# Kernel tuning notes

Measured on AMD Instinct MI355X. Metric: run time of the kernel, lower is better.

The kernel has to match this reference:

```python
import jax, jax.numpy as jnp
import numpy as np


def _conv(x, w, b):
    # NCHW conv with 'same' padding derived from kernel size (matches nn.Conv2d padding=k//2)
    ph, pw = w.shape[2] // 2, w.shape[3] // 2
    y = jax.lax.conv_general_dilated(
        x, w, window_strides=(1, 1), padding=[(ph, ph), (pw, pw)],
        dimension_numbers=("NCHW", "OIHW", "NCHW"))
    return y + b[None, :, None, None]


def _attn(q, k, v):
    # q,k,v: [N,C,H,W]; spatial self-attention over S=H*W positions
    N, C, H, W = q.shape
    S = H * W
    qf = q.reshape(N, C, S)
    kf = k.reshape(N, C, S)
    vf = v.reshape(N, C, S)
    scores = jnp.einsum("ncs,nct->nst", qf, kf) / jnp.sqrt(jnp.asarray(C, qf.dtype))
    a = jax.nn.softmax(scores, axis=-1)
    z = jnp.einsum("nst,nct->ncs", a, vf)
    return z.reshape(N, C, H, W)


def setup_inputs() -> dict:
    key = jax.random.key(0)
    ks = jax.random.split(key, 14)
    B, T, Ci, Hd, H, W = 4, 10, 1, 64, 32, 32
    sc = 0.05
    return {
        "x": jax.random.uniform(ks[0], (B, T, Ci, H, W), jnp.float32),
        # SAConvLSTMCell main conv: (Ci+Hd) -> 4*Hd, 3x3
        "w_conv": jax.random.normal(ks[1], (4 * Hd, Ci + Hd, 3, 3), jnp.float32) * sc,
        "b_conv": jax.random.normal(ks[2], (4 * Hd,), jnp.float32) * sc,
        # SA conv_h: Hd -> 3*Hd, 1x1
        "w_h": jax.random.normal(ks[3], (3 * Hd, Hd, 1, 1), jnp.float32) * sc,
        "b_h": jax.random.normal(ks[4], (3 * Hd,), jnp.float32) * sc,
        # SA conv_m: Hd -> 2*Hd, 1x1
        "w_m": jax.random.normal(ks[5], (2 * Hd, Hd, 1, 1), jnp.float32) * sc,
        "b_m": jax.random.normal(ks[6], (2 * Hd,), jnp.float32) * sc,
        # SA conv_z: 2*Hd -> Hd, 1x1
        "w_z": jax.random.normal(ks[7], (Hd, 2 * Hd, 1, 1), jnp.float32) * sc,
        "b_z": jax.random.normal(ks[8], (Hd,), jnp.float32) * sc,
        # SA conv_output: 2*Hd -> 3*Hd, 3x3
        "w_sa": jax.random.normal(ks[9], (3 * Hd, 2 * Hd, 3, 3), jnp.float32) * sc,
        "b_sa": jax.random.normal(ks[10], (3 * Hd,), jnp.float32) * sc,
        # conv_out: Hd -> Ci, 1x1
        "w_co": jax.random.normal(ks[11], (Ci, Hd, 1, 1), jnp.float32) * sc,
        "b_co": jax.random.normal(ks[12], (Ci,), jnp.float32) * sc,
        "future_frames": 10,
    }


def reference(x, w_conv, b_conv, w_h, b_h, w_m, b_m, w_z, b_z,
              w_sa, b_sa, w_co, b_co, future_frames):
    B, T, Ci, H, W = x.shape
    Hd = w_conv.shape[0] // 4

    def cell(xt, h, c, m):
        cc = _conv(jnp.concatenate([xt, h], axis=1), w_conv, b_conv)
        i, f, o, g = jnp.split(cc, 4, axis=1)
        c_new = jax.nn.sigmoid(f) * c + jax.nn.sigmoid(i) * jnp.tanh(g)
        h_cur = jax.nn.sigmoid(o) * jnp.tanh(c_new)
        # spatial self-attention memory update
        hq, hk, hv = jnp.split(_conv(h_cur, w_h, b_h), 3, axis=1)
        mk, mv = jnp.split(_conv(m, w_m, b_m), 2, axis=1)
        Zh = _attn(hq, hk, hv)
        Zm = _attn(hq, mk, mv)
        Z = _conv(jnp.concatenate([Zh, Zm], axis=1), w_z, b_z)
        i2, g2, o2 = jnp.split(_conv(jnp.concatenate([Z, h_cur], axis=1), w_sa, b_sa), 3, axis=1)
        i2 = jax.nn.sigmoid(i2)
        m_new = i2 * jnp.tanh(g2) + (1.0 - i2) * m
        h_new = jax.nn.sigmoid(o2) * m_new
        return h_new, c_new, m_new

    z = jnp.zeros((B, Hd, H, W), x.dtype)
    state0 = (z, z, z)

    def enc_step(carry, xt):
        h, c, m = carry
        return cell(xt, h, c, m), None

    (h, c, m), _ = jax.lax.scan(enc_step, state0, jnp.moveaxis(x, 1, 0))

    # first decoder input: raw conv_out(h) (no sigmoid, per the original code path)
    inp0 = _conv(h, w_co, b_co)

    def dec_step(carry, _):
        h, c, m, inp = carry
        h, c, m = cell(inp, h, c, m)
        pred = jax.nn.sigmoid(_conv(h, w_co, b_co))
        return (h, c, m, pred), pred

    _, preds = jax.lax.scan(dec_step, (h, c, m, inp0), None, length=future_frames)
    return jnp.moveaxis(preds, 0, 1)  # [B, future_frames, Ci, H, W]
```

## Files before the change

kernel.cpp:

```cpp
#include <hip/hip_runtime.h>
#include <math.h>

#define SS 1024

typedef unsigned short u16;
typedef __attribute__((ext_vector_type(8))) __bf16 bf16x8;
typedef __attribute__((ext_vector_type(4))) float f32x4;

#define MFMA(a,b,c) __builtin_amdgcn_mfma_f32_16x16x32_bf16(a,b,c,0,0,0)

__device__ __forceinline__ float sigm(float x){ return 1.f/(1.f+__expf(-x)); }
__device__ __forceinline__ u16 f2b(float x){ return __builtin_bit_cast(u16,(__bf16)x); }
__device__ __forceinline__ float b2f(u16 u){ return (float)__builtin_bit_cast(__bf16,u); }
__device__ __forceinline__ bf16x8 ldb8(const u16* p){ return *(const bf16x8*)p; }
__device__ __forceinline__ void st4b(u16* p, const f32x4 v){
  union { u16 u[4]; uint2 w; } t;
  t.u[0]=f2b(v[0]); t.u[1]=f2b(v[1]); t.u[2]=f2b(v[2]); t.u[3]=f2b(v[3]);
  *(uint2*)p = t.w;
}

__global__ __launch_bounds__(256) void k_prep(
    const float* __restrict__ wconv, const float* __restrict__ wh,
    const float* __restrict__ wm, const float* __restrict__ wz,
    const float* __restrict__ wsa,
    u16* __restrict__ Wg, u16* __restrict__ Whm,
    u16* __restrict__ Wzp, u16* __restrict__ Wsap)
{
  const int idx = blockIdx.x*256 + threadIdx.x;
  if (idx < 155648) {
    const int step = idx >> 13, co = (idx >> 5) & 255, j = idx & 31;
    float v = 0.f;
    if (step < 18) {
      const int tap = step >> 1, ci = 1 + (step & 1)*32 + j;
      v = wconv[co*585 + ci*9 + tap];
    } else if (j < 9) {
      v = wconv[co*585 + j];
    }
    Wg[idx] = f2b(v);
    return;
  }
  int l = idx - 155648;
  if (l < 20480) {
    const int step = l / 10240, row = (l >> 5) % 320, j = l & 31;
    const int ci = step*32 + j;
    const float v = (row < 192) ? wh[row*64+ci]*(row < 64 ? 0.125f : 1.f)
                                : wm[(row-192)*64+ci];
    Whm[l] = f2b(v);
    return;
  }
  l -= 20480;
  if (l < 8192) {
    const int step = l >> 11, co = (l >> 5) & 63, j = l & 31;
    Wzp[l] = f2b(wz[co*128 + step*32 + j]);
    return;
  }
  l -= 8192;
  if (l < 221184) {
    const int step = l / 6144, co = (l >> 5) % 192, j = l & 31;
    const int tap = step >> 2, ci = (step & 3)*32 + j;
    Wsap[l] = f2b(wsa[(co*128+ci)*9 + tap]);
  }
}

__global__ __launch_bounds__(256) void k_A(
    const u16* __restrict__ hTb, const float* __restrict__ xsrc, int xbs,
    const u16* __restrict__ Wg, const float* __restrict__ bconv,
    float* __restrict__ cT, u16* __restrict__ xcat,
    const u16* __restrict__ mTb, const u16* __restrict__ Whm,
    const float* __restrict__ bh, const float* __restrict__ bm,
    u16* __restrict__ qT, u16* __restrict__ kT, u16* __restrict__ mkT,
    u16* __restrict__ vC, u16* __restrict__ mvC)
{
  __shared__ u16 hcl[16][72];
  const int b = blockIdx.y, s0 = blockIdx.x*16;
  const int tid = threadIdx.x, wid = tid>>6, lane = tid&63, gl = lane>>4, n = lane&15;
  const u16* hb = hTb + (size_t)b*SS*64;
  const int s = s0 + n, y = s>>5, x = s&31;
  f32x4 acc[4];
#pragma unroll
  for (int g4 = 0; g4 < 4; ++g4) {
    const int co = g4*64 + wid*16 + gl*4;
    acc[g4] = (f32x4){ bconv[co], bconv[co+1], bconv[co+2], bconv[co+3] };
  }
  bf16x8 xb;
  {
    union { u16 u[8]; bf16x8 v; } t;
#pragma unroll
    for (int j = 0; j < 8; ++j) t.u[j] = 0;
    if (gl == 0) {
#pragma unroll
      for (int j = 0; j < 8; ++j) {
        const int dy = j/3 - 1, dx = j%3 - 1;
        if ((unsigned)(y+dy) < 32u && (unsigned)(x+dx) < 32u)
          t.u[j] = f2b(xsrc[b*xbs + s + dy*32 + dx]);
      }
    } else if (gl == 1) {
      if (y+1 < 32 && x+1 < 32) t.u[0] = f2b(xsrc[b*xbs + s + 33]);
    }
    xb = t.v;
  }
#pragma unroll
  for (int step = 0; step < 18; ++step) {
    const int tap = step>>1, half = step&1;
    const int dy = tap/3 - 1, dx = tap%3 - 1;
    const bool ok = ((unsigned)(y+dy) < 32u) & ((unsigned)(x+dx) < 32u);
    const int sc = ok ? (s + dy*32 + dx) : s;
    bf16x8 bv = ldb8(hb + (size_t)sc*64 + half*32 + gl*8);
    bv = ok ? bv : (bf16x8){};
#pragma unroll
    for (int g4 = 0; g4 < 4; ++g4) {
      const bf16x8 a = ldb8(Wg + step*8192 + (g4*64 + wid*16 + n)*32 + gl*8);
      acc[g4] = MFMA(a, bv, acc[g4]);
    }
  }
#pragma unroll
  for (int g4 = 0; g4 < 4; ++g4) {
    const bf16x8 a = ldb8(Wg + 18*8192 + (g4*64 + wid*16 + n)*32 + gl*8);
    acc[g4] = MFMA(a, xb, acc[g4]);
  }
  const int hd0 = wid*16 + gl*4;
  {
    float* cp = cT + ((size_t)b*SS + s)*64 + hd0;
    f32x4 cv = *(f32x4*)cp, hcv;
#pragma unroll
    for (int rr = 0; rr < 4; ++rr) {
      const float cn = sigm(acc[1][rr])*cv[rr] + sigm(acc[0][rr])*tanhf(acc[3][rr]);
      cv[rr] = cn;
      hcv[rr] = sigm(acc[2][rr])*tanhf(cn);
    }
    *(f32x4*)cp = cv;
    st4b(xcat + ((size_t)b*SS + s)*128 + 64 + hd0, hcv);
    st4b(&hcl[n][hd0], hcv);
  }
  __syncthreads();
  const int r0 = wid*16, cb = r0 + gl*4;
  f32x4 a1[5];
  a1[0] = (f32x4){ bh[cb]*0.125f, bh[cb+1]*0.125f, bh[cb+2]*0.125f, bh[cb+3]*0.125f };
  a1[1] = (f32x4){ bh[64+cb], bh[64+cb+1], bh[64+cb+2], bh[64+cb+3] };
  a1[2] = (f32x4){ bh[128+cb], bh[128+cb+1], bh[128+cb+2], bh[128+cb+3] };
  a1[3] = (f32x4){ bm[cb], bm[cb+1], bm[cb+2], bm[cb+3] };
  a1[4] = (f32x4){ bm[64+cb], bm[64+cb+1], bm[64+cb+2], bm[64+cb+3] };
#pragma unroll
  for (int step = 0; step < 2; ++step) {
    const bf16x8 bhc = ldb8(&hcl[n][step*32 + gl*8]);
    const bf16x8 bmm = ldb8(mTb + ((size_t)b*SS+s)*64 + step*32 + gl*8);
#pragma unroll
    for (int tt = 0; tt < 5; ++tt) {
      const bf16x8 a = ldb8(Whm + step*10240 + (tt*64 + r0 + n)*32 + gl*8);
      a1[tt] = MFMA(a, tt < 3 ? bhc : bmm, a1[tt]);
    }
  }
  const size_t ps = ((size_t)b*SS + s)*64 + cb;
  st4b(qT + ps, a1[0]);
  st4b(kT + ps, a1[1]);
  st4b(mkT + ps, a1[3]);
#pragma unroll
  for (int rr = 0; rr < 4; ++rr) {
    vC[((size_t)b*64 + cb + rr)*SS + s] = f2b(a1[2][rr]);
    mvC[((size_t)b*64 + cb + rr)*SS + s] = f2b(a1[4][rr]);
  }
}

__global__ __launch_bounds__(256) void k_B(
    const u16* __restrict__ qT, const u16* __restrict__ kT,
    const u16* __restrict__ mkT, const u16* __restrict__ vC,
    const u16* __restrict__ mvC,
    const u16* __restrict__ Wzp, const float* __restrict__ bz,
    u16* __restrict__ xcat)
{
  __shared__ u16 ldsP[4*16*72];
  __shared__ float oS[2][16][65];
  __shared__ float mS[2][16], lS[2][16];
  __shared__ u16 zbuf[16][136];
  const int tid = threadIdx.x, wid = tid>>6, lane = tid&63, gl = lane>>4, n = lane&15;
  const int b = blockIdx.z ? 0 : blockIdx.y, s0 = blockIdx.x*16;
  const int at = wid & 1, kv = wid >> 1;
  const u16* qb = qT + (size_t)b*SS*64;
  const u16* kb = (at ? mkT : kT) + (size_t)b*SS*64;
  const u16* vb = (at ? mvC : vC) + (size_t)b*64*SS;
  const bf16x8 bq0 = ldb8(qb + (size_t)(s0+n)*64 + gl*8);
  const bf16x8 bq1 = ldb8(qb + (size_t)(s0+n)*64 + 32 + gl*8);
  f32x4 o[4];
#pragma unroll
  for (int ct = 0; ct < 4; ++ct) o[ct] = (f32x4){0.f,0.f,0.f,0.f};
  float mrun = -1e30f, lrun = 0.f;
  u16* pb = ldsP + wid*1152 + n*72;

  for (int step = 0; step < 8; ++step) {
    const int t0 = kv*512 + step*64;
    f32x4 st4[4];
#pragma unroll
    for (int tt = 0; tt < 4; ++tt) {
      const u16* kr = kb + (size_t)(t0 + tt*16 + n)*64;
      f32x4 a = {0.f,0.f,0.f,0.f};
      a = MFMA(ldb8(kr + gl*8), bq0, a);
      a = MFMA(ldb8(kr + 32 + gl*8), bq1, a);
      st4[tt] = a;
    }
    float mt = -1e30f;
#pragma unroll
    for (int tt = 0; tt < 4; ++tt)
#pragma unroll
      for (int rr = 0; rr < 4; ++rr) mt = fmaxf(mt, st4[tt][rr]);
    mt = fmaxf(mt, __shfl_xor(mt, 16));
    mt = fmaxf(mt, __shfl_xor(mt, 32));
    const float mnew = fmaxf(mrun, mt);
    const float f = __expf(mrun - mnew);
    float ps = 0.f;
#pragma unroll
    for (int tt = 0; tt < 4; ++tt) {
      const float p0e = __expf(st4[tt][0]-mnew), p1e = __expf(st4[tt][1]-mnew);
      const float p2e = __expf(st4[tt][2]-mnew), p3e = __expf(st4[tt][3]-mnew);
      ps += (p0e + p1e) + (p2e + p3e);
      *(unsigned*)(pb + tt*16 + gl*4)     = (unsigned)f2b(p0e) | ((unsigned)f2b(p1e)<<16);
      *(unsigned*)(pb + tt*16 + gl*4 + 2) = (unsigned)f2b(p2e) | ((unsigned)f2b(p3e)<<16);
    }
    ps += __shfl_xor(ps, 16);
    ps += __shfl_xor(ps, 32);
    lrun = lrun*f + ps;
    mrun = mnew;
    float fr[4];
#pragma unroll
    for (int rr = 0; rr < 4; ++rr) fr[rr] = __shfl(f, gl*4 + rr);
#pragma unroll
    for (int ct = 0; ct < 4; ++ct)
#pragma unroll
      for (int rr = 0; rr < 4; ++rr) o[ct][rr] *= fr[rr];
    const bf16x8 pa0 = ldb8(pb + gl*8);
    const bf16x8 pa1 = ldb8(pb + 32 + gl*8);
#pragma unroll
    for (int ct = 0; ct < 4; ++ct) {
      const u16* vr = vb + (size_t)(ct*16 + n)*SS + t0;
      o[ct] = MFMA(pa0, ldb8(vr + gl*8), o[ct]);
      o[ct] = MFMA(pa1, ldb8(vr + 32 + gl*8), o[ct]);
    }
  }
  if (kv == 1) {
#pragma unroll
    for (int ct = 0; ct < 4; ++ct)
#pragma unroll
      for (int rr = 0; rr < 4; ++rr) oS[at][gl*4+rr][ct*16+n] = o[ct][rr];
    if (gl == 0) { mS[at][n] = mrun; lS[at][n] = lrun; }
  }
  __syncthreads();
  if (kv == 0) {
    const float m1 = mS[at][n], l1 = lS[at][n];
    const float mm = fmaxf(mrun, m1);
    const float e0 = __expf(mrun - mm), e1 = __expf(m1 - mm);
    const float inv = 1.f / (lrun*e0 + l1*e1);
    const float a0 = e0*inv, a1v = e1*inv;
    float f0r[4], f1r[4];
#pragma unroll
    for (int rr = 0; rr < 4; ++rr) {
      f0r[rr] = __shfl(a0, gl*4 + rr);
      f1r[rr] = __shfl(a1v, gl*4 + rr);
    }
#pragma unroll
    for (int ct = 0; ct < 4; ++ct)
#pragma unroll
      for (int rr = 0; rr < 4; ++rr)
        zbuf[gl*4+rr][at*64 + ct*16 + n] =
            f2b(o[ct][rr]*f0r[rr] + oS[at][gl*4+rr][ct*16+n]*f1r[rr]);
  }
  __syncthreads();
  const int co = wid*16 + gl*4;
  f32x4 acc = (f32x4){ bz[co], bz[co+1], bz[co+2], bz[co+3] };
#pragma unroll
  for (int qq = 0; qq < 4; ++qq) {
    const bf16x8 bv = ldb8(&zbuf[n][qq*32 + gl*8]);
    const bf16x8 a = ldb8(Wzp + qq*2048 + (wid*16 + n)*32 + gl*8);
    acc = MFMA(a, bv, acc);
  }
  st4b(xcat + ((size_t)b*SS + s0 + n)*128 + co, acc);
}

__global__ __launch_bounds__(256) void k_C(
    const u16* __restrict__ xcat, const u16* __restrict__ Wsap,
    const float* __restrict__ bsa,
    float* __restrict__ mT, u16* __restrict__ mTb, u16* __restrict__ hTb,
    const float* __restrict__ wco, const float* __restrict__ bco,
    float* __restrict__ inp, float* __restrict__ out, int mode, int j)
{
  __shared__ float pool[16][17];
  const int b = blockIdx.y, s0 = blockIdx.x*16;
  const int tid = threadIdx.x, wid = tid>>6, lane = tid&63, gl = lane>>4, n = lane&15;
  const int hd0 = wid*16 + gl*4;
  const int s = s0 + n, y = s>>5, x = s&31;
  f32x4 acc[3];
#pragma unroll
  for (int i = 0; i < 3; ++i) {
    const int co = i*64 + hd0;
    acc[i] = (f32x4){ bsa[co], bsa[co+1], bsa[co+2], bsa[co+3] };
  }
#pragma unroll
  for (int step = 0; step < 36; ++step) {
    const int tap = step>>2, qq = step&3;
    const int dy = tap/3 - 1, dx = tap%3 - 1;
    const bool ok = ((unsigned)(y+dy) < 32u) & ((unsigned)(x+dx) < 32u);
    const int sc = ok ? (s + dy*32 + dx) : s;
    bf16x8 bv = ldb8(xcat + ((size_t)b*SS + sc)*128 + qq*32 + gl*8);
    bv = ok ? bv : (bf16x8){};
#pragma unroll
    for (int i = 0; i < 3; ++i) {
      const bf16x8 a = ldb8(Wsap + step*6144 + (i*64 + wid*16 + n)*32 + gl*8);
      acc[i] = MFMA(a, bv, acc[i]);
    }
  }
  float* mp = mT + ((size_t)b*SS + s)*64 + hd0;
  f32x4 mv4 = *(f32x4*)mp, hv;
#pragma unroll
  for (int rr = 0; rr < 4; ++rr) {
    const float i2 = sigm(acc[0][rr]);
    const float mn = i2*tanhf(acc[1][rr]) + (1.f - i2)*mv4[rr];
    mv4[rr] = mn;
    hv[rr] = sigm(acc[2][rr])*mn;
  }
  *(f32x4*)mp = mv4;
  st4b(mTb + ((size_t)b*SS + s)*64 + hd0, mv4);
  st4b(hTb + ((size_t)b*SS + s)*64 + hd0, hv);
  if (mode >= 0) {
    pool[n][wid*4 + gl] = hv[0]*wco[hd0] + hv[1]*wco[hd0+1]
                        + hv[2]*wco[hd0+2] + hv[3]*wco[hd0+3];
    __syncthreads();
    if (tid < 16) {
      float v = bco[0];
#pragma unroll
      for (int i = 0; i < 16; ++i) v += pool[tid][i];
      const int sp = s0 + tid;
      if (mode == 1) {
        v = sigm(v);
        out[((size_t)b*10 + j)*SS + sp] = v;
      }
      inp[b*SS + sp] = v;
    }
  }
}

extern "C" void kernel_launch(void* const* d_in, const int* in_sizes, int n_in,
                              void* d_out, int out_size, void* d_ws, size_t ws_size,
                              hipStream_t stream) {
  const float* x      = (const float*)d_in[0];
  const float* w_conv = (const float*)d_in[1];
  const float* b_conv = (const float*)d_in[2];
  const float* w_h    = (const float*)d_in[3];
  const float* b_h    = (const float*)d_in[4];
  const float* w_m    = (const float*)d_in[5];
  const float* b_m    = (const float*)d_in[6];
  const float* w_z    = (const float*)d_in[7];
  const float* b_z    = (const float*)d_in[8];
  const float* w_sa   = (const float*)d_in[9];
  const float* b_sa   = (const float*)d_in[10];
  const float* w_co   = (const float*)d_in[11];
  const float* b_co   = (const float*)d_in[12];
  float* out = (float*)d_out;

  float* ws  = (float*)d_ws;
  float* cT  = ws;
  float* mT  = ws + 262144;
  float* inp = ws + 524288;
  u16* ub   = (u16*)(ws + 528384);
  u16* hTb  = ub;
  u16* mTb  = ub + 262144;
  u16* xcat = ub + 524288;
  u16* qT   = ub + 1048576;
  u16* kT   = ub + 1310720;
  u16* mkT  = ub + 1572864;
  u16* vC   = ub + 1835008;
  u16* mvC  = ub + 2097152;
  u16* Wg   = ub + 2359296;
  u16* Whm  = ub + 2514944;
  u16* Wzp  = ub + 2535424;
  u16* Wsap = ub + 2543616;

  hipMemsetAsync(ws, 0, (size_t)524288*4, stream);
  hipMemsetAsync(hTb, 0, (size_t)524288*2, stream);
  k_prep<<<dim3(1584), 256, 0, stream>>>(w_conv, w_h, w_m, w_z, w_sa, Wg, Whm, Wzp, Wsap);

  auto cell = [&](const float* xsrc, int xbs, int mode, int j) {
    k_A<<<dim3(64,4), 256, 0, stream>>>(hTb, xsrc, xbs, Wg, b_conv, cT, xcat,
                                        mTb, Whm, b_h, b_m, qT, kT, mkT, vC, mvC);
    k_B<<<dim3(64,4), 256, 0, stream>>>(qT, kT, mkT, vC, mvC, Wzp, b_z, xcat);
    k_C<<<dim3(64,4), 256, 0, stream>>>(xcat, Wsap, b_sa, mT, mTb, hTb,
                                        w_co, b_co, inp, out, mode, j);
  };

  for (int t = 0; t < 10; ++t)
    cell(x + (size_t)t*SS, 10*SS, (t == 9) ? 0 : -1, 0);
  for (int j = 0; j < 10; ++j)
    cell(inp, SS, 1, j);
}
```

Baseline: 1.072 ms.

## Fuse all cell steps into one persistent kernel with grid-wide barriers

Replaces the 61 separate launches (prep plus three kernels per timestep over 20 steps) with a single persistent kernel of 256 blocks. Phases are separated by a software grid barrier built on atomics. Weight packing and state zeroing move into the same kernel. The aim is to remove per-launch overhead and inter-kernel gaps. In exchange, all blocks must be co-resident, which holds with 256 blocks on this GPU, and the spin-wait barrier itself costs something on every phase.

```diff
diff --git a/kernel.cpp b/kernel.cpp
--- a/kernel.cpp
+++ b/kernel.cpp
@@ -2,6 +2,7 @@
 #include <math.h>
 
 #define SS 1024
+#define NBLK 256u
 
 typedef unsigned short u16;
 typedef __attribute__((ext_vector_type(8))) __bf16 bf16x8;
@@ -19,320 +20,341 @@
   *(uint2*)p = t.w;
 }
 
-__global__ __launch_bounds__(256) void k_prep(
-    const float* __restrict__ wconv, const float* __restrict__ wh,
-    const float* __restrict__ wm, const float* __restrict__ wz,
-    const float* __restrict__ wsa,
+__device__ __forceinline__ void gbar(unsigned* cnt, unsigned* gen) {
+  __syncthreads();
+  if (threadIdx.x == 0) {
+    const unsigned g = __hip_atomic_load(gen, __ATOMIC_RELAXED, __HIP_MEMORY_SCOPE_AGENT);
+    if (__hip_atomic_fetch_add(cnt, 1u, __ATOMIC_ACQ_REL, __HIP_MEMORY_SCOPE_AGENT) == NBLK - 1u) {
+      __hip_atomic_store(cnt, 0u, __ATOMIC_RELAXED, __HIP_MEMORY_SCOPE_AGENT);
+      __hip_atomic_store(gen, g + 1u, __ATOMIC_RELEASE, __HIP_MEMORY_SCOPE_AGENT);
+    } else {
+      while (__hip_atomic_load(gen, __ATOMIC_ACQUIRE, __HIP_MEMORY_SCOPE_AGENT) == g)
+        __builtin_amdgcn_s_sleep(2);
+    }
+  }
+  __syncthreads();
+}
+
+__global__ __launch_bounds__(256, 1) void k_all(
+    const float* __restrict__ x,
+    const float* __restrict__ wconv, const float* __restrict__ bconv,
+    const float* __restrict__ wh,    const float* __restrict__ bh,
+    const float* __restrict__ wm,    const float* __restrict__ bm,
+    const float* __restrict__ wz,    const float* __restrict__ bz,
+    const float* __restrict__ wsa,   const float* __restrict__ bsa,
+    const float* __restrict__ wco,   const float* __restrict__ bco,
+    float* __restrict__ cT, float* __restrict__ mT, float* __restrict__ inp,
+    unsigned* __restrict__ bar,
+    u16* __restrict__ hTb, u16* __restrict__ mTb, u16* __restrict__ xcat,
+    u16* __restrict__ qT, u16* __restrict__ kT, u16* __restrict__ mkT,
+    u16* __restrict__ vC, u16* __restrict__ mvC,
     u16* __restrict__ Wg, u16* __restrict__ Whm,
-    u16* __restrict__ Wzp, u16* __restrict__ Wsap)
-{
-  const int idx = blockIdx.x*256 + threadIdx.x;
-  if (idx < 155648) {
-    const int step = idx >> 13, co = (idx >> 5) & 255, j = idx & 31;
-    float v = 0.f;
-    if (step < 18) {
-      const int tap = step >> 1, ci = 1 + (step & 1)*32 + j;
-      v = wconv[co*585 + ci*9 + tap];
-    } else if (j < 9) {
-      v = wconv[co*585 + j];
-    }
-    Wg[idx] = f2b(v);
-    return;
-  }
-  int l = idx - 155648;
-  if (l < 20480) {
-    const int step = l / 10240, row = (l >> 5) % 320, j = l & 31;
-    const int ci = step*32 + j;
-    const float v = (row < 192) ? wh[row*64+ci]*(row < 64 ? 0.125f : 1.f)
-                                : wm[(row-192)*64+ci];
-    Whm[l] = f2b(v);
-    return;
-  }
-  l -= 20480;
-  if (l < 8192) {
-    const int step = l >> 11, co = (l >> 5) & 63, j = l & 31;
-    Wzp[l] = f2b(wz[co*128 + step*32 + j]);
-    return;
-  }
-  l -= 8192;
-  if (l < 221184) {
-    const int step = l / 6144, co = (l >> 5) % 192, j = l & 31;
-    const int tap = step >> 2, ci = (step & 3)*32 + j;
-    Wsap[l] = f2b(wsa[(co*128+ci)*9 + tap]);
-  }
-}
-
-__global__ __launch_bounds__(256) void k_A(
-    const u16* __restrict__ hTb, const float* __restrict__ xsrc, int xbs,
-    const u16* __restrict__ Wg, const float* __restrict__ bconv,
-    float* __restrict__ cT, u16* __restrict__ xcat,
-    const u16* __restrict__ mTb, const u16* __restrict__ Whm,
-    const float* __restrict__ bh, const float* __restrict__ bm,
-    u16* __restrict__ qT, u16* __restrict__ kT, u16* __restrict__ mkT,
-    u16* __restrict__ vC, u16* __restrict__ mvC)
+    u16* __restrict__ Wzp, u16* __restrict__ Wsap,
+    float* __restrict__ out)
 {
   __shared__ u16 hcl[16][72];
-  const int b = blockIdx.y, s0 = blockIdx.x*16;
-  const int tid = threadIdx.x, wid = tid>>6, lane = tid&63, gl = lane>>4, n = lane&15;
-  const u16* hb = hTb + (size_t)b*SS*64;
-  const int s = s0 + n, y = s>>5, x = s&31;
-  f32x4 acc[4];
-#pragma unroll
-  for (int g4 = 0; g4 < 4; ++g4) {
-    const int co = g4*64 + wid*16 + gl*4;
-    acc[g4] = (f32x4){ bconv[co], bconv[co+1], bconv[co+2], bconv[co+3] };
-  }
-  bf16x8 xb;
-  {
-    union { u16 u[8]; bf16x8 v; } t;
-#pragma unroll
-    for (int j = 0; j < 8; ++j) t.u[j] = 0;
-    if (gl == 0) {
-#pragma unroll
-      for (int j = 0; j < 8; ++j) {
-        const int dy = j/3 - 1, dx = j%3 - 1;
-        if ((unsigned)(y+dy) < 32u && (unsigned)(x+dx) < 32u)
-          t.u[j] = f2b(xsrc[b*xbs + s + dy*32 + dx]);
-      }
-    } else if (gl == 1) {
-      if (y+1 < 32 && x+1 < 32) t.u[0] = f2b(xsrc[b*xbs + s + 33]);
-    }
-    xb = t.v;
-  }
-#pragma unroll
-  for (int step = 0; step < 18; ++step) {
-    const int tap = step>>1, half = step&1;
-    const int dy = tap/3 - 1, dx = tap%3 - 1;
-    const bool ok = ((unsigned)(y+dy) < 32u) & ((unsigned)(x+dx) < 32u);
-    const int sc = ok ? (s + dy*32 + dx) : s;
-    bf16x8 bv = ldb8(hb + (size_t)sc*64 + half*32 + gl*8);
-    bv = ok ? bv : (bf16x8){};
-#pragma unroll
-    for (int g4 = 0; g4 < 4; ++g4) {
-      const bf16x8 a = ldb8(Wg + step*8192 + (g4*64 + wid*16 + n)*32 + gl*8);
-      acc[g4] = MFMA(a, bv, acc[g4]);
-    }
-  }
-#pragma unroll
-  for (int g4 = 0; g4 < 4; ++g4) {
-    const bf16x8 a = ldb8(Wg + 18*8192 + (g4*64 + wid*16 + n)*32 + gl*8);
-    acc[g4] = MFMA(a, xb, acc[g4]);
-  }
-  const int hd0 = wid*16 + gl*4;
-  {
-    float* cp = cT + ((size_t)b*SS + s)*64 + hd0;
-    f32x4 cv = *(f32x4*)cp, hcv;
-#pragma unroll
-    for (int rr = 0; rr < 4; ++rr) {
-      const float cn = sigm(acc[1][rr])*cv[rr] + sigm(acc[0][rr])*tanhf(acc[3][rr]);
-      cv[rr] = cn;
-      hcv[rr] = sigm(acc[2][rr])*tanhf(cn);
-    }
-    *(f32x4*)cp = cv;
-    st4b(xcat + ((size_t)b*SS + s)*128 + 64 + hd0, hcv);
-    st4b(&hcl[n][hd0], hcv);
-  }
-  __syncthreads();
-  const int r0 = wid*16, cb = r0 + gl*4;
-  f32x4 a1[5];
-  a1[0] = (f32x4){ bh[cb]*0.125f, bh[cb+1]*0.125f, bh[cb+2]*0.125f, bh[cb+3]*0.125f };
-  a1[1] = (f32x4){ bh[64+cb], bh[64+cb+1], bh[64+cb+2], bh[64+cb+3] };
-  a1[2] = (f32x4){ bh[128+cb], bh[128+cb+1], bh[128+cb+2], bh[128+cb+3] };
-  a1[3] = (f32x4){ bm[cb], bm[cb+1], bm[cb+2], bm[cb+3] };
-  a1[4] = (f32x4){ bm[64+cb], bm[64+cb+1], bm[64+cb+2], bm[64+cb+3] };
-#pragma unroll
-  for (int step = 0; step < 2; ++step) {
-    const bf16x8 bhc = ldb8(&hcl[n][step*32 + gl*8]);
-    const bf16x8 bmm = ldb8(mTb + ((size_t)b*SS+s)*64 + step*32 + gl*8);
-#pragma unroll
-    for (int tt = 0; tt < 5; ++tt) {
-      const bf16x8 a = ldb8(Whm + step*10240 + (tt*64 + r0 + n)*32 + gl*8);
-      a1[tt] = MFMA(a, tt < 3 ? bhc : bmm, a1[tt]);
-    }
-  }
-  const size_t ps = ((size_t)b*SS + s)*64 + cb;
-  st4b(qT + ps, a1[0]);
-  st4b(kT + ps, a1[1]);
-  st4b(mkT + ps, a1[3]);
-#pragma unroll
-  for (int rr = 0; rr < 4; ++rr) {
-    vC[((size_t)b*64 + cb + rr)*SS + s] = f2b(a1[2][rr]);
-    mvC[((size_t)b*64 + cb + rr)*SS + s] = f2b(a1[4][rr]);
-  }
-}
-
-__global__ __launch_bounds__(256) void k_B(
-    const u16* __restrict__ qT, const u16* __restrict__ kT,
-    const u16* __restrict__ mkT, const u16* __restrict__ vC,
-    const u16* __restrict__ mvC,
-    const u16* __restrict__ Wzp, const float* __restrict__ bz,
-    u16* __restrict__ xcat)
-{
   __shared__ u16 ldsP[4*16*72];
   __shared__ float oS[2][16][65];
   __shared__ float mS[2][16], lS[2][16];
   __shared__ u16 zbuf[16][136];
+  __shared__ float pool[16][17];
+
   const int tid = threadIdx.x, wid = tid>>6, lane = tid&63, gl = lane>>4, n = lane&15;
-  const int b = blockIdx.z ? 0 : blockIdx.y, s0 = blockIdx.x*16;
-  const int at = wid & 1, kv = wid >> 1;
-  const u16* qb = qT + (size_t)b*SS*64;
-  const u16* kb = (at ? mkT : kT) + (size_t)b*SS*64;
-  const u16* vb = (at ? mvC : vC) + (size_t)b*64*SS;
-  const bf16x8 bq0 = ldb8(qb + (size_t)(s0+n)*64 + gl*8);
-  const bf16x8 bq1 = ldb8(qb + (size_t)(s0+n)*64 + 32 + gl*8);
-  f32x4 o[4];
-#pragma unroll
-  for (int ct = 0; ct < 4; ++ct) o[ct] = (f32x4){0.f,0.f,0.f,0.f};
-  float mrun = -1e30f, lrun = 0.f;
-  u16* pb = ldsP + wid*1152 + n*72;
-
-  for (int step = 0; step < 8; ++step) {
-    const int t0 = kv*512 + step*64;
-    f32x4 st4[4];
-#pragma unroll
-    for (int tt = 0; tt < 4; ++tt) {
-      const u16* kr = kb + (size_t)(t0 + tt*16 + n)*64;
-      f32x4 a = {0.f,0.f,0.f,0.f};
-      a = MFMA(ldb8(kr + gl*8), bq0, a);
-      a = MFMA(ldb8(kr + 32 + gl*8), bq1, a);
-      st4[tt] = a;
-    }
-    float mt = -1e30f;
-#pragma unroll
-    for (int tt = 0; tt < 4; ++tt)
-#pragma unroll
-      for (int rr = 0; rr < 4; ++rr) mt = fmaxf(mt, st4[tt][rr]);
-    mt = fmaxf(mt, __shfl_xor(mt, 16));
-    mt = fmaxf(mt, __shfl_xor(mt, 32));
-    const float mnew = fmaxf(mrun, mt);
-    const float f = __expf(mrun - mnew);
-    float ps = 0.f;
-#pragma unroll
-    for (int tt = 0; tt < 4; ++tt) {
-      const float p0e = __expf(st4[tt][0]-mnew), p1e = __expf(st4[tt][1]-mnew);
-      const float p2e = __expf(st4[tt][2]-mnew), p3e = __expf(st4[tt][3]-mnew);
-      ps += (p0e + p1e) + (p2e + p3e);
-      *(unsigned*)(pb + tt*16 + gl*4)     = (unsigned)f2b(p0e) | ((unsigned)f2b(p1e)<<16);
-      *(unsigned*)(pb + tt*16 + gl*4 + 2) = (unsigned)f2b(p2e) | ((unsigned)f2b(p3e)<<16);
-    }
-    ps += __shfl_xor(ps, 16);
-    ps += __shfl_xor(ps, 32);
-    lrun = lrun*f + ps;
-    mrun = mnew;
-    float fr[4];
-#pragma unroll
-    for (int rr = 0; rr < 4; ++rr) fr[rr] = __shfl(f, gl*4 + rr);
-#pragma unroll
-    for (int ct = 0; ct < 4; ++ct)
-#pragma unroll
-      for (int rr = 0; rr < 4; ++rr) o[ct][rr] *= fr[rr];
-    const bf16x8 pa0 = ldb8(pb + gl*8);
-    const bf16x8 pa1 = ldb8(pb + 32 + gl*8);
-#pragma unroll
-    for (int ct = 0; ct < 4; ++ct) {
-      const u16* vr = vb + (size_t)(ct*16 + n)*SS + t0;
-      o[ct] = MFMA(pa0, ldb8(vr + gl*8), o[ct]);
-      o[ct] = MFMA(pa1, ldb8(vr + 32 + gl*8), o[ct]);
+  const int sb = blockIdx.x, b = blockIdx.y, s0 = sb*16;
+  const int flatb = b*64 + sb;
+  const int s = s0 + n, y = s>>5, xx = s&31;
+
+  for (int i = tid; i < 1024; i += 256) {
+    const size_t o4 = ((size_t)b*SS + s0 + (i>>6))*64 + (i&63);
+    cT[o4] = 0.f; mT[o4] = 0.f; hTb[o4] = 0; mTb[o4] = 0;
+  }
+  for (int i = tid; i < 1584; i += 256) {
+    const int idx = flatb*1584 + i;
+    if (idx < 155648) {
+      const int step = idx >> 13, co = (idx >> 5) & 255, jj = idx & 31;
+      float v = 0.f;
+      if (step < 18) {
+        const int tap = step >> 1, ci = 1 + (step & 1)*32 + jj;
+        v = wconv[co*585 + ci*9 + tap];
+      } else if (jj < 9) {
+        v = wconv[co*585 + jj];
+      }
+      Wg[idx] = f2b(v);
+    } else {
+      int l = idx - 155648;
+      if (l < 20480) {
+        const int step = l / 10240, row = (l >> 5) % 320, jj = l & 31;
+        const int ci = step*32 + jj;
+        const float v = (row < 192) ? wh[row*64+ci]*(row < 64 ? 0.125f : 1.f)
+                                    : wm[(row-192)*64+ci];
+        Whm[l] = f2b(v);
+      } else {
+        l -= 20480;
+        if (l < 8192) {
+          const int step = l >> 11, co = (l >> 5) & 63, jj = l & 31;
+          Wzp[l] = f2b(wz[co*128 + step*32 + jj]);
+        } else {
+          l -= 8192;
+          const int step = l / 6144, co = (l >> 5) % 192, jj = l & 31;
+          const int tap = step >> 2, ci = (step & 3)*32 + jj;
+          Wsap[l] = f2b(wsa[(co*128+ci)*9 + tap]);
+        }
+      }
     }
   }
-  if (kv == 1) {
-#pragma unroll
-    for (int ct = 0; ct < 4; ++ct)
-#pragma unroll
-      for (int rr = 0; rr < 4; ++rr) oS[at][gl*4+rr][ct*16+n] = o[ct][rr];
-    if (gl == 0) { mS[at][n] = mrun; lS[at][n] = lrun; }
-  }
-  __syncthreads();
-  if (kv == 0) {
-    const float m1 = mS[at][n], l1 = lS[at][n];
-    const float mm = fmaxf(mrun, m1);
-    const float e0 = __expf(mrun - mm), e1 = __expf(m1 - mm);
-    const float inv = 1.f / (lrun*e0 + l1*e1);
-    const float a0 = e0*inv, a1v = e1*inv;
-    float f0r[4], f1r[4];
-#pragma unroll
-    for (int rr = 0; rr < 4; ++rr) {
-      f0r[rr] = __shfl(a0, gl*4 + rr);
-      f1r[rr] = __shfl(a1v, gl*4 + rr);
+  gbar(bar, bar+1);
+
+#pragma unroll 1
+  for (int t = 0; t < 20; ++t) {
+    const float* xs = (t < 10) ? (x + (size_t)t*SS) : inp;
+    const int xbs = (t < 10) ? 10*SS : SS;
+
+    {
+      const u16* hb = hTb + (size_t)b*SS*64;
+      f32x4 acc[4];
+#pragma unroll
+      for (int g4 = 0; g4 < 4; ++g4) {
+        const int co = g4*64 + wid*16 + gl*4;
+        acc[g4] = (f32x4){ bconv[co], bconv[co+1], bconv[co+2], bconv[co+3] };
+      }
+      bf16x8 xb;
+      {
+        union { u16 u[8]; bf16x8 v; } tt;
+#pragma unroll
+        for (int jj = 0; jj < 8; ++jj) tt.u[jj] = 0;
+        if (gl == 0) {
+#pragma unroll
+          for (int jj = 0; jj < 8; ++jj) {
+            const int dy = jj/3 - 1, dx = jj%3 - 1;
+            if ((unsigned)(y+dy) < 32u && (unsigned)(xx+dx) < 32u)
+              tt.u[jj] = f2b(xs[b*xbs + s + dy*32 + dx]);
+          }
+        } else if (gl == 1) {
+          if (y+1 < 32 && xx+1 < 32) tt.u[0] = f2b(xs[b*xbs + s + 33]);
+        }
+        xb = tt.v;
+      }
+#pragma unroll
+      for (int step = 0; step < 18; ++step) {
+        const int tap = step>>1, half = step&1;
+        const int dy = tap/3 - 1, dx = tap%3 - 1;
+        const bool ok = ((unsigned)(y+dy) < 32u) & ((unsigned)(xx+dx) < 32u);
+        const int sc = ok ? (s + dy*32 + dx) : s;
+        bf16x8 bv = ldb8(hb + (size_t)sc*64 + half*32 + gl*8);
+        bv = ok ? bv : (bf16x8){};
+#pragma unroll
+        for (int g4 = 0; g4 < 4; ++g4) {
+          const bf16x8 a = ldb8(Wg + step*8192 + (g4*64 + wid*16 + n)*32 + gl*8);
+          acc[g4] = MFMA(a, bv, acc[g4]);
+        }
+      }
+#pragma unroll
+      for (int g4 = 0; g4 < 4; ++g4) {
+        const bf16x8 a = ldb8(Wg + 18*8192 + (g4*64 + wid*16 + n)*32 + gl*8);
+        acc[g4] = MFMA(a, xb, acc[g4]);
+      }
+      const int hd0 = wid*16 + gl*4;
+      {
+        float* cp = cT + ((size_t)b*SS + s)*64 + hd0;
+        f32x4 cv = *(f32x4*)cp, hcv;
+#pragma unroll
+        for (int rr = 0; rr < 4; ++rr) {
+          const float cn = sigm(acc[1][rr])*cv[rr] + sigm(acc[0][rr])*tanhf(acc[3][rr]);
+          cv[rr] = cn;
+          hcv[rr] = sigm(acc[2][rr])*tanhf(cn);
+        }
+        *(f32x4*)cp = cv;
+        st4b(xcat + ((size_t)b*SS + s)*128 + 64 + hd0, hcv);
+        st4b(&hcl[n][hd0], hcv);
+      }
+      __syncthreads();
+      const int r0 = wid*16, cb = r0 + gl*4;
+      f32x4 a1[5];
+      a1[0] = (f32x4){ bh[cb]*0.125f, bh[cb+1]*0.125f, bh[cb+2]*0.125f, bh[cb+3]*0.125f };
+      a1[1] = (f32x4){ bh[64+cb], bh[64+cb+1], bh[64+cb+2], bh[64+cb+3] };
+      a1[2] = (f32x4){ bh[128+cb], bh[128+cb+1], bh[128+cb+2], bh[128+cb+3] };
+      a1[3] = (f32x4){ bm[cb], bm[cb+1], bm[cb+2], bm[cb+3] };
+      a1[4] = (f32x4){ bm[64+cb], bm[64+cb+1], bm[64+cb+2], bm[64+cb+3] };
+#pragma unroll
+      for (int step = 0; step < 2; ++step) {
+        const bf16x8 bhc = ldb8(&hcl[n][step*32 + gl*8]);
+        const bf16x8 bmm = ldb8(mTb + ((size_t)b*SS+s)*64 + step*32 + gl*8);
+#pragma unroll
+        for (int tt = 0; tt < 5; ++tt) {
+          const bf16x8 a = ldb8(Whm + step*10240 + (tt*64 + r0 + n)*32 + gl*8);
+          a1[tt] = MFMA(a, tt < 3 ? bhc : bmm, a1[tt]);
+        }
+      }
+      const size_t ps = ((size_t)b*SS + s)*64 + cb;
+      st4b(qT + ps, a1[0]);
+      st4b(kT + ps, a1[1]);
+      st4b(mkT + ps, a1[3]);
+#pragma unroll
+      for (int rr = 0; rr < 4; ++rr) {
+        vC[((size_t)b*64 + cb + rr)*SS + s] = f2b(a1[2][rr]);
+        mvC[((size_t)b*64 + cb + rr)*SS + s] = f2b(a1[4][rr]);
+      }
     }
-#pragma unroll
-    for (int ct = 0; ct < 4; ++ct)
-#pragma unroll
-      for (int rr = 0; rr < 4; ++rr)
-        zbuf[gl*4+rr][at*64 + ct*16 + n] =
-            f2b(o[ct][rr]*f0r[rr] + oS[at][gl*4+rr][ct*16+n]*f1r[rr]);
-  }
-  __syncthreads();
-  const int co = wid*16 + gl*4;
-  f32x4 acc = (f32x4){ bz[co], bz[co+1], bz[co+2], bz[co+3] };
-#pragma unroll
-  for (int qq = 0; qq < 4; ++qq) {
-    const bf16x8 bv = ldb8(&zbuf[n][qq*32 + gl*8]);
-    const bf16x8 a = ldb8(Wzp + qq*2048 + (wid*16 + n)*32 + gl*8);
-    acc = MFMA(a, bv, acc);
-  }
-  st4b(xcat + ((size_t)b*SS + s0 + n)*128 + co, acc);
-}
-
-__global__ __launch_bounds__(256) void k_C(
-    const u16* __restrict__ xcat, const u16* __restrict__ Wsap,
-    const float* __restrict__ bsa,
-    float* __restrict__ mT, u16* __restrict__ mTb, u16* __restrict__ hTb,
-    const float* __restrict__ wco, const float* __restrict__ bco,
-    float* __restrict__ inp, float* __restrict__ out, int mode, int j)
-{
-  __shared__ float pool[16][17];
-  const int b = blockIdx.y, s0 = blockIdx.x*16;
-  const int tid = threadIdx.x, wid = tid>>6, lane = tid&63, gl = lane>>4, n = lane&15;
-  const int hd0 = wid*16 + gl*4;
-  const int s = s0 + n, y = s>>5, x = s&31;
-  f32x4 acc[3];
-#pragma unroll
-  for (int i = 0; i < 3; ++i) {
-    const int co = i*64 + hd0;
-    acc[i] = (f32x4){ bsa[co], bsa[co+1], bsa[co+2], bsa[co+3] };
-  }
-#pragma unroll
-  for (int step = 0; step < 36; ++step) {
-    const int tap = step>>2, qq = step&3;
-    const int dy = tap/3 - 1, dx = tap%3 - 1;
-    const bool ok = ((unsigned)(y+dy) < 32u) & ((unsigned)(x+dx) < 32u);
-    const int sc = ok ? (s + dy*32 + dx) : s;
-    bf16x8 bv = ldb8(xcat + ((size_t)b*SS + sc)*128 + qq*32 + gl*8);
-    bv = ok ? bv : (bf16x8){};
-#pragma unroll
-    for (int i = 0; i < 3; ++i) {
-      const bf16x8 a = ldb8(Wsap + step*6144 + (i*64 + wid*16 + n)*32 + gl*8);
-      acc[i] = MFMA(a, bv, acc[i]);
+    gbar(bar, bar+1);
+
+    {
+      const int at = wid & 1, kv = wid >> 1;
+      const u16* qb = qT + (size_t)b*SS*64;
+      const u16* kb = (at ? mkT : kT) + (size_t)b*SS*64;
+      const u16* vb = (at ? mvC : vC) + (size_t)b*64*SS;
+      const bf16x8 bq0 = ldb8(qb + (size_t)(s0+n)*64 + gl*8);
+      const bf16x8 bq1 = ldb8(qb + (size_t)(s0+n)*64 + 32 + gl*8);
+      f32x4 o[4];
+#pragma unroll
+      for (int ct = 0; ct < 4; ++ct) o[ct] = (f32x4){0.f,0.f,0.f,0.f};
+      float mrun = -1e30f, lrun = 0.f;
+      u16* pb = ldsP + wid*1152 + n*72;
+#pragma unroll 1
+      for (int step = 0; step < 8; ++step) {
+        const int t0 = kv*512 + step*64;
+        f32x4 st4[4];
+#pragma unroll
+        for (int tt = 0; tt < 4; ++tt) {
+          const u16* kr = kb + (size_t)(t0 + tt*16 + n)*64;
+          f32x4 a = {0.f,0.f,0.f,0.f};
+          a = MFMA(ldb8(kr + gl*8), bq0, a);
+          a = MFMA(ldb8(kr + 32 + gl*8), bq1, a);
+          st4[tt] = a;
+        }
+        float mt = -1e30f;
+#pragma unroll
+        for (int tt = 0; tt < 4; ++tt)
+#pragma unroll
+          for (int rr = 0; rr < 4; ++rr) mt = fmaxf(mt, st4[tt][rr]);
+        mt = fmaxf(mt, __shfl_xor(mt, 16));
+        mt = fmaxf(mt, __shfl_xor(mt, 32));
+        const float mnew = fmaxf(mrun, mt);
+        const float f = __expf(mrun - mnew);
+        float ps = 0.f;
+#pragma unroll
+        for (int tt = 0; tt < 4; ++tt) {
+          const float p0e = __expf(st4[tt][0]-mnew), p1e = __expf(st4[tt][1]-mnew);
+          const float p2e = __expf(st4[tt][2]-mnew), p3e = __expf(st4[tt][3]-mnew);
+          ps += (p0e + p1e) + (p2e + p3e);
+          *(unsigned*)(pb + tt*16 + gl*4)     = (unsigned)f2b(p0e) | ((unsigned)f2b(p1e)<<16);
+          *(unsigned*)(pb + tt*16 + gl*4 + 2) = (unsigned)f2b(p2e) | ((unsigned)f2b(p3e)<<16);
+        }
+        ps += __shfl_xor(ps, 16);
+        ps += __shfl_xor(ps, 32);
+        lrun = lrun*f + ps;
+        mrun = mnew;
+        float fr[4];
+#pragma unroll
+        for (int rr = 0; rr < 4; ++rr) fr[rr] = __shfl(f, gl*4 + rr);
+#pragma unroll
+        for (int ct = 0; ct < 4; ++ct)
+#pragma unroll
+          for (int rr = 0; rr < 4; ++rr) o[ct][rr] *= fr[rr];
+        const bf16x8 pa0 = ldb8(pb + gl*8);
+        const bf16x8 pa1 = ldb8(pb + 32 + gl*8);
+#pragma unroll
+        for (int ct = 0; ct < 4; ++ct) {
+          const u16* vr = vb + (size_t)(ct*16 + n)*SS + t0;
+          o[ct] = MFMA(pa0, ldb8(vr + gl*8), o[ct]);
+          o[ct] = MFMA(pa1, ldb8(vr + 32 + gl*8), o[ct]);
+        }
+      }
+      if (kv == 1) {
+#pragma unroll
+        for (int ct = 0; ct < 4; ++ct)
+#pragma unroll
+          for (int rr = 0; rr < 4; ++rr) oS[at][gl*4+rr][ct*16+n] = o[ct][rr];
+        if (gl == 0) { mS[at][n] = mrun; lS[at][n] = lrun; }
+      }
+      __syncthreads();
+      if (kv == 0) {
+        const float m1 = mS[at][n], l1 = lS[at][n];
+        const float mm = fmaxf(mrun, m1);
+        const float e0 = __expf(mrun - mm), e1 = __expf(m1 - mm);
+        const float inv = 1.f / (lrun*e0 + l1*e1);
+        const float a0 = e0*inv, a1v = e1*inv;
+        float f0r[4], f1r[4];
+#pragma unroll
+        for (int rr = 0; rr < 4; ++rr) {
+          f0r[rr] = __shfl(a0, gl*4 + rr);
+          f1r[rr] = __shfl(a1v, gl*4 + rr);
+        }
+#pragma unroll
+        for (int ct = 0; ct < 4; ++ct)
+#pragma unroll
+          for (int rr = 0; rr < 4; ++rr)
+            zbuf[gl*4+rr][at*64 + ct*16 + n] =
+                f2b(o[ct][rr]*f0r[rr] + oS[at][gl*4+rr][ct*16+n]*f1r[rr]);
+      }
+      __syncthreads();
+      const int co = wid*16 + gl*4;
+      f32x4 acc = (f32x4){ bz[co], bz[co+1], bz[co+2], bz[co+3] };
+#pragma unroll
+      for (int qq = 0; qq < 4; ++qq) {
+        const bf16x8 bv = ldb8(&zbuf[n][qq*32 + gl*8]);
+        const bf16x8 a = ldb8(Wzp + qq*2048 + (wid*16 + n)*32 + gl*8);
+        acc = MFMA(a, bv, acc);
+      }
+      st4b(xcat + ((size_t)b*SS + s0 + n)*128 + co, acc);
+      __syncthreads();
     }
-  }
-  float* mp = mT + ((size_t)b*SS + s)*64 + hd0;
-  f32x4 mv4 = *(f32x4*)mp, hv;
-#pragma unroll
-  for (int rr = 0; rr < 4; ++rr) {
-    const float i2 = sigm(acc[0][rr]);
-    const float mn = i2*tanhf(acc[1][rr]) + (1.f - i2)*mv4[rr];
-    mv4[rr] = mn;
-    hv[rr] = sigm(acc[2][rr])*mn;
-  }
-  *(f32x4*)mp = mv4;
-  st4b(mTb + ((size_t)b*SS + s)*64 + hd0, mv4);
-  st4b(hTb + ((size_t)b*SS + s)*64 + hd0, hv);
-  if (mode >= 0) {
-    pool[n][wid*4 + gl] = hv[0]*wco[hd0] + hv[1]*wco[hd0+1]
-                        + hv[2]*wco[hd0+2] + hv[3]*wco[hd0+3];
-    __syncthreads();
-    if (tid < 16) {
-      float v = bco[0];
-#pragma unroll
-      for (int i = 0; i < 16; ++i) v += pool[tid][i];
-      const int sp = s0 + tid;
-      if (mode == 1) {
-        v = sigm(v);
-        out[((size_t)b*10 + j)*SS + sp] = v;
-      }
-      inp[b*SS + sp] = v;
+    gbar(bar, bar+1);
+
+    {
+      const int mode = (t < 9) ? -1 : (t == 9 ? 0 : 1);
+      const int j = t - 10;
+      const int hd0 = wid*16 + gl*4;
+      f32x4 acc[3];
+#pragma unroll
+      for (int i = 0; i < 3; ++i) {
+        const int co = i*64 + hd0;
+        acc[i] = (f32x4){ bsa[co], bsa[co+1], bsa[co+2], bsa[co+3] };
+      }
+#pragma unroll
+      for (int step = 0; step < 36; ++step) {
+        const int tap = step>>2, qq = step&3;
+        const int dy = tap/3 - 1, dx = tap%3 - 1;
+        const bool ok = ((unsigned)(y+dy) < 32u) & ((unsigned)(xx+dx) < 32u);
+        const int sc = ok ? (s + dy*32 + dx) : s;
+        bf16x8 bv = ldb8(xcat + ((size_t)b*SS + sc)*128 + qq*32 + gl*8);
+        bv = ok ? bv : (bf16x8){};
+#pragma unroll
+        for (int i = 0; i < 3; ++i) {
+          const bf16x8 a = ldb8(Wsap + step*6144 + (i*64 + wid*16 + n)*32 + gl*8);
+          acc[i] = MFMA(a, bv, acc[i]);
+        }
+      }
+      float* mp = mT + ((size_t)b*SS + s)*64 + hd0;
+      f32x4 mv4 = *(f32x4*)mp, hv;
+#pragma unroll
+      for (int rr = 0; rr < 4; ++rr) {
+        const float i2 = sigm(acc[0][rr]);
+        const float mn = i2*tanhf(acc[1][rr]) + (1.f - i2)*mv4[rr];
+        mv4[rr] = mn;
+        hv[rr] = sigm(acc[2][rr])*mn;
+      }
+      *(f32x4*)mp = mv4;
+      st4b(mTb + ((size_t)b*SS + s)*64 + hd0, mv4);
+      st4b(hTb + ((size_t)b*SS + s)*64 + hd0, hv);
+      if (mode >= 0) {
+        pool[n][wid*4 + gl] = hv[0]*wco[hd0] + hv[1]*wco[hd0+1]
+                            + hv[2]*wco[hd0+2] + hv[3]*wco[hd0+3];
+        __syncthreads();
+        if (tid < 16) {
+          float v = bco[0];
+#pragma unroll
+          for (int i = 0; i < 16; ++i) v += pool[tid][i];
+          const int sp = s0 + tid;
+          if (mode == 1) {
+            v = sigm(v);
+            out[((size_t)b*10 + j)*SS + sp] = v;
+          }
+          inp[b*SS + sp] = v;
+        }
+        __syncthreads();
+      }
     }
+    gbar(bar, bar+1);
   }
 }
 
@@ -358,7 +380,8 @@
   float* cT  = ws;
   float* mT  = ws + 262144;
   float* inp = ws + 524288;
-  u16* ub   = (u16*)(ws + 528384);
+  unsigned* bar = (unsigned*)(ws + 528384);
+  u16* ub   = (u16*)(ws + 528448);
   u16* hTb  = ub;
   u16* mTb  = ub + 262144;
   u16* xcat = ub + 524288;
@@ -372,20 +395,10 @@
   u16* Wzp  = ub + 2535424;
   u16* Wsap = ub + 2543616;
 
-  hipMemsetAsync(ws, 0, (size_t)524288*4, stream);
-  hipMemsetAsync(hTb, 0, (size_t)524288*2, stream);
-  k_prep<<<dim3(1584), 256, 0, stream>>>(w_conv, w_h, w_m, w_z, w_sa, Wg, Whm, Wzp, Wsap);
-
-  auto cell = [&](const float* xsrc, int xbs, int mode, int j) {
-    k_A<<<dim3(64,4), 256, 0, stream>>>(hTb, xsrc, xbs, Wg, b_conv, cT, xcat,
-                                        mTb, Whm, b_h, b_m, qT, kT, mkT, vC, mvC);
-    k_B<<<dim3(64,4), 256, 0, stream>>>(qT, kT, mkT, vC, mvC, Wzp, b_z, xcat);
-    k_C<<<dim3(64,4), 256, 0, stream>>>(xcat, Wsap, b_sa, mT, mTb, hTb,
-                                        w_co, b_co, inp, out, mode, j);
-  };
-
-  for (int t = 0; t < 10; ++t)
-    cell(x + (size_t)t*SS, 10*SS, (t == 9) ? 0 : -1, 0);
-  for (int j = 0; j < 10; ++j)
-    cell(inp, SS, 1, j);
+  hipMemsetAsync(bar, 0, 8, stream);
+
+  k_all<<<dim3(64,4), 256, 0, stream>>>(
+      x, w_conv, b_conv, w_h, b_h, w_m, b_m, w_z, b_z, w_sa, b_sa, w_co, b_co,
+      cT, mT, inp, bar, hTb, mTb, xcat, qT, kT, mkT, vC, mvC,
+      Wg, Whm, Wzp, Wsap, out);
 }
```

After: 3.687 ms. 244% more time.
